# Kernel tuning notes

Hardware: AMD Instinct MI355X
Metric: run time of the kernel (lower is better)

Reference implementation:

```python
import jax, jax.numpy as jnp
import numpy as np

H_DIM = 256
N_HEADS = 8
HALF = H_DIM // 2

def _lin(x, W, b):
    # torch nn.Linear: y = x @ W.T + b
    y = x @ W.T
    return y + b if b is not None else y

def setup_inputs() -> dict:
    key = jax.random.key(0)
    ks = jax.random.split(key, 16)
    s = 0.02
    d = {
        'x': jax.random.normal(ks[0], (16, H_DIM, 32, 32), jnp.float32),
        'q1_w': jax.random.normal(ks[1], (HALF, HALF), jnp.float32) * s,
        'q1_b': jnp.zeros((HALF,), jnp.float32),
        'q2_w': jax.random.normal(ks[2], (HALF, HALF), jnp.float32) * s,
        'q2_b': jnp.zeros((HALF,), jnp.float32),
        'k1_w': jax.random.normal(ks[3], (HALF, HALF), jnp.float32) * s,
        'k1_b': jnp.zeros((HALF,), jnp.float32),
        'k2_w': jax.random.normal(ks[4], (HALF, HALF), jnp.float32) * s,
        'k2_b': jnp.zeros((HALF,), jnp.float32),
        'v1_w': jax.random.normal(ks[5], (HALF, HALF), jnp.float32) * s,
        'v1_b': jnp.zeros((HALF,), jnp.float32),
        'v2_w': jax.random.normal(ks[6], (HALF, HALF), jnp.float32) * s,
        'v2_b': jnp.zeros((HALF,), jnp.float32),
        'proj1_w': jax.random.normal(ks[7], (HALF, HALF), jnp.float32) * s,
        'proj1_b': jnp.zeros((HALF,), jnp.float32),
        'proj2_w': jax.random.normal(ks[8], (HALF, HALF), jnp.float32) * s,
        'proj2_b': jnp.zeros((HALF,), jnp.float32),
        'logit_scale': jnp.log(10.0 * jnp.ones((N_HEADS, 1, 1), jnp.float32)),
        'mlp_w1': jax.random.normal(ks[9], (128, 2), jnp.float32) * s,
        'mlp_b1': jnp.zeros((128,), jnp.float32),
        'mlp_w2': jax.random.normal(ks[10], (N_HEADS, 128), jnp.float32) * s,
    }
    return d

def _rel_pos_index(h, w):
    # static (numpy) relative position index, shape [N, N]
    ch, cw = np.meshgrid(np.arange(h), np.arange(w), indexing='ij')
    coords = np.stack([ch.reshape(-1), cw.reshape(-1)])  # [2, N]
    rel = coords[:, :, None] - coords[:, None, :]         # [2, N, N]
    rel = rel.transpose(1, 2, 0)
    rel[:, :, 0] += h - 1
    rel[:, :, 1] += w - 1
    return rel[:, :, 0] * (2 * w - 1) + rel[:, :, 1]

def _forward(x, q1_w, q1_b, q2_w, q2_b, k1_w, k1_b, k2_w, k2_b,
             v1_w, v1_b, v2_w, v2_b, proj1_w, proj1_b, proj2_w, proj2_b,
             logit_scale, mlp_w1, mlp_b1, mlp_w2):
    b, c, h, w = x.shape
    N = h * w
    nh = N_HEADS
    hd = c // nh
    x3 = jnp.transpose(x, (0, 2, 3, 1)).reshape(b, N, c)
    x0, x1 = x3[..., :c // 2], x3[..., c // 2:]

    def qkv(W0, b0, W1, b1):
        t = jnp.concatenate([x0 + _lin(x0, W0, b0), x1 + _lin(x1, W1, b1)], axis=-1)
        return t.reshape(b, N, nh, hd).transpose(0, 2, 1, 3)  # [b, nh, N, hd]

    q = qkv(q1_w, q1_b, q2_w, q2_b)
    k = qkv(k1_w, k1_b, k2_w, k2_b)
    v = qkv(v1_w, v1_b, v2_w, v2_b)

    eps = 1e-12
    qn = q / jnp.maximum(jnp.linalg.norm(q, axis=-1, keepdims=True), eps)
    kn = k / jnp.maximum(jnp.linalg.norm(k, axis=-1, keepdims=True), eps)
    attn = jnp.einsum('bhnd,bhmd->bhnm', qn, kn)  # cosine similarity
    scale = jnp.exp(jnp.minimum(logit_scale, jnp.log(1.0 / 0.01)))  # [nh,1,1]
    attn = attn * scale[None]

    # continuous relative-position bias (CPB) table via small MLP
    rch = jnp.arange(-(h - 1), h, dtype=jnp.float32) / (h - 1 + 1e-8)
    rcw = jnp.arange(-(w - 1), w, dtype=jnp.float32) / (w - 1 + 1e-8)
    gh, gw = jnp.meshgrid(rch, rcw, indexing='ij')
    tab = jnp.stack([gh, gw], axis=-1) * 3.2               # [2h-1, 2w-1, 2]
    tab = jnp.sign(tab) * (1.0 - jnp.exp(-jnp.abs(tab)))
    tab = jax.nn.relu(_lin(tab, mlp_w1, mlp_b1))
    tab = _lin(tab, mlp_w2, None).reshape(-1, nh)          # [(2h-1)(2w-1), nh]

    idx = jnp.asarray(_rel_pos_index(h, w))                # [N, N]
    bias = tab[idx.reshape(-1)].reshape(N, N, nh).transpose(2, 0, 1)
    bias = 16.0 * jax.nn.sigmoid(bias)
    attn = attn + bias[None]

    attn = jax.nn.softmax(attn, axis=-1)
    out = jnp.einsum('bhnm,bhmd->bhnd', attn, v).transpose(0, 2, 1, 3).reshape(b, N, c)
    o0, o1 = out[..., :c // 2], out[..., c // 2:]
    out = jnp.concatenate([_lin(o0, proj1_w, proj1_b), _lin(o1, proj2_w, proj2_b)], axis=-1)
    return out.reshape(b, h, w, c).transpose(0, 3, 1, 2)

def reference(x, q1_w, q1_b, q2_w, q2_b, k1_w, k1_b, k2_w, k2_b,
              v1_w, v1_b, v2_w, v2_b, proj1_w, proj1_b, proj2_w, proj2_b,
              logit_scale, mlp_w1, mlp_b1, mlp_w2):
    return _forward(x, q1_w, q1_b, q2_w, q2_b, k1_w, k1_b, k2_w, k2_b,
                    v1_w, v1_b, v2_w, v2_b, proj1_w, proj1_b, proj2_w, proj2_b,
                    logit_scale, mlp_w1, mlp_b1, mlp_w2)
```

## Files before the change

### kernel.cpp

```cpp
#include <hip/hip_runtime.h>
#include <cmath>


typedef _Float16 half_t;
typedef __attribute__((ext_vector_type(4))) _Float16 half4;
typedef __attribute__((ext_vector_type(8))) _Float16 half8;
typedef __attribute__((ext_vector_type(4))) float float4v;

static __device__ __forceinline__ float4v mfma16(half8 a, half8 b, float4v c) {
  return __builtin_amdgcn_mfma_f32_16x16x32_f16(a, b, c, 0, 0, 0);
}

struct PtrArr8 { const float* p[8]; };

__global__ __launch_bounds__(256) void bias_mlp(const float* __restrict__ w1,
                                                const float* __restrict__ b1,
                                                const float* __restrict__ w2,
                                                const float* __restrict__ ls,
                                                float* __restrict__ tabh2) {
  __shared__ float sw1[256];
  __shared__ float sb1[128];
  __shared__ float sw2[1024];
  int t = threadIdx.x;
  sw1[t] = w1[t];
  if (t < 128) sb1[t] = b1[t];
  for (int i = t; i < 1024; i += 256) sw2[i] = w2[i];
  __syncthreads();
  int p = blockIdx.x * 256 + t;
  if (p >= 3969) return;
  int ph = p / 63, pw = p % 63;
  float t0 = (float)(ph - 31) * (3.2f / 31.0f);
  float t1 = (float)(pw - 31) * (3.2f / 31.0f);
  t0 = copysignf(1.0f - __expf(-fabsf(t0)), t0);
  t1 = copysignf(1.0f - __expf(-fabsf(t1)), t1);
  float acc[8];
#pragma unroll
  for (int hh = 0; hh < 8; hh++) acc[hh] = 0.0f;
  for (int j = 0; j < 128; j++) {
    float hj = fmaxf(0.0f, t0 * sw1[2 * j] + t1 * sw1[2 * j + 1] + sb1[j]);
#pragma unroll
    for (int hh = 0; hh < 8; hh++) acc[hh] += hj * sw2[hh * 128 + j];
  }
  const float L2E = 1.44269504f;
#pragma unroll
  for (int hh = 0; hh < 8; hh++) {
    float scale = __expf(fminf(ls[hh], 4.6051702f));
    float c14 = 14.0f - (scale + 16.0f) * L2E;
    float bias = 16.0f / (1.0f + __expf(-acc[hh]));
    tabh2[hh * 3969 + p] = bias * L2E + c14;
  }
}

__global__ __launch_bounds__(256) void qkv_mfma(
    const float* __restrict__ x, PtrArr8 wsrc, PtrArr8 bsrc,
    const float* __restrict__ lscale, half_t* __restrict__ qf,
    half_t* __restrict__ kf, half_t* __restrict__ vf) {
  __shared__ half_t wb[128 * 136];
  __shared__ half_t tbuf[128 * 68];
  int t = threadIdx.x;
  int lane = t & 63, wv = t >> 6, l = lane & 15, quad = lane >> 4;
  int hf = blockIdx.y;
  int m0 = blockIdx.x * 64;
  int b = m0 >> 10, n0 = m0 & 1023;

  half8 afr[4];
  {
    const float* xb = x + (size_t)b * 256 * 1024 + n0 + wv * 16 + l;
#pragma unroll
    for (int ks = 0; ks < 4; ks++) {
      int kbase = hf * 128 + ks * 32 + quad * 8;
      half8 a;
#pragma unroll
      for (int j = 0; j < 8; j++)
        a[j] = (half_t)xb[(size_t)(kbase + j) * 1024];
      afr[ks] = a;
    }
  }

  for (int op = 0; op < 3; op++) {
    int combo = op * 2 + hf;
    const float* wg = nullptr;
    const float* bg = nullptr;
#pragma unroll
    for (int i = 0; i < 6; i++)
      if (i == combo) { wg = wsrc.p[i]; bg = bsrc.p[i]; }
    __syncthreads();
#pragma unroll
    for (int i = 0; i < 16; i++) {
      int flat = (t + 256 * i) * 4;
      int row = flat >> 7, col = flat & 127;
      float4 w = *(const float4*)(wg + flat);
      half4 h;
      h[0] = (half_t)(w.x + (col == row ? 1.0f : 0.0f));
      h[1] = (half_t)(w.y + (col + 1 == row ? 1.0f : 0.0f));
      h[2] = (half_t)(w.z + (col + 2 == row ? 1.0f : 0.0f));
      h[3] = (half_t)(w.w + (col + 3 == row ? 1.0f : 0.0f));
      *(half4*)(wb + row * 136 + col) = h;
    }
    __syncthreads();

    float4v acc[8];
#pragma unroll
    for (int ng = 0; ng < 8; ng++) {
      float4v c = {0.f, 0.f, 0.f, 0.f};
#pragma unroll
      for (int ks = 0; ks < 4; ks++) {
        half8 bfrag =
            *(const half8*)(wb + (ng * 16 + l) * 136 + ks * 32 + quad * 8);
        c = mfma16(afr[ks], bfrag, c);
      }
      acc[ng] = c;
    }
#pragma unroll
    for (int ng = 0; ng < 8; ng++) {
      float bb = bg[ng * 16 + l];
#pragma unroll
      for (int r2 = 0; r2 < 4; r2++) acc[ng][r2] += bb;
    }
    if (op < 2) {
#pragma unroll
      for (int hg = 0; hg < 4; hg++) {
        float sc = 1.0f;
        if (op == 0)
          sc = __expf(fminf(lscale[hf * 4 + hg], 4.6051702f)) * 1.44269504f;
#pragma unroll
        for (int r2 = 0; r2 < 4; r2++) {
          float ss = acc[2 * hg][r2] * acc[2 * hg][r2] +
                     acc[2 * hg + 1][r2] * acc[2 * hg + 1][r2];
          ss += __shfl_xor(ss, 1, 64);
          ss += __shfl_xor(ss, 2, 64);
          ss += __shfl_xor(ss, 4, 64);
          ss += __shfl_xor(ss, 8, 64);
          float rn = sc / fmaxf(sqrtf(ss), 1e-12f);
          acc[2 * hg][r2] *= rn;
          acc[2 * hg + 1][r2] *= rn;
        }
      }
#pragma unroll
      for (int ng = 0; ng < 8; ng++)
#pragma unroll
        for (int r2 = 0; r2 < 4; r2++)
          tbuf[(wv * 16 + quad * 4 + r2) * 132 + ng * 16 + l] =
              (half_t)acc[ng][r2];
      __syncthreads();
      half_t* dst = (op == 0) ? qf : kf;
#pragma unroll
      for (int i = 0; i < 4; i++) {
        int idx = t + 256 * i;
        int row = idx >> 4, colc = (idx & 15) * 8;
        half8 vv = *(const half8*)(tbuf + row * 132 + colc);
        int head = hf * 4 + (colc >> 5), d = colc & 31;
        *(half8*)(dst + (((size_t)b * 8 + head) * 1024 + n0 + row) * 32 + d) =
            vv;
      }
    } else {
#pragma unroll
      for (int ng = 0; ng < 8; ng++) {
        int col = ng * 16 + l;
        half4 hv;
#pragma unroll
        for (int r2 = 0; r2 < 4; r2++) hv[r2] = (half_t)acc[ng][r2];
        *(half4*)(tbuf + col * 68 + wv * 16 + quad * 4) = hv;
      }
      __syncthreads();
#pragma unroll
      for (int i = 0; i < 16; i++) {
        int idx = t + 256 * i;
        int col = idx >> 5, rp = idx & 31;
        unsigned int val = *(const unsigned int*)(tbuf + col * 68 + rp * 2);
        int head = hf * 4 + (col >> 5);
        int d = col & 31;
        *(unsigned int*)((char*)vf +
                         (((((size_t)b * 8 + head) * 32 + d) * 1024) + n0 +
                          rp * 2) * 2) = val;
      }
    }
  }
}

__global__ __launch_bounds__(256) void attn_mfma(
    const half_t* __restrict__ qf, const half_t* __restrict__ kf,
    const half_t* __restrict__ vf, const float* __restrict__ tabh2,
    half_t* __restrict__ ao) {
  __shared__ float sb2[35 * 63];
  __shared__ half_t pa[4 * 16 * 80];

  int t = threadIdx.x;
  int lane = t & 63, wv = t >> 6, l = lane & 15, quad = lane >> 4;
  int qo = blockIdx.x, h = blockIdx.y, b = blockIdx.z;
  size_t bh = (size_t)b * 8 + h;
  const half_t* kbase = kf + bh * 1024 * 32;
  const half_t* vbase = vf + bh * 32 * 1024;

  for (int i = t; i < 2205; i += 256)
    sb2[i] = tabh2[h * 3969 + qo * 252 + i];

  int row0 = qo * 128 + wv * 32;
  half8 qfr[2];
#pragma unroll
  for (int s = 0; s < 2; s++)
    qfr[s] =
        *(const half8*)(qf + (bh * 1024 + row0 + s * 16 + l) * 32 + quad * 8);

  float4v o0[2], o1[2];
  float run_l[2];
#pragma unroll
  for (int s = 0; s < 2; s++) {
    o0[s] = (float4v){0.f, 0.f, 0.f, 0.f};
    o1[s] = (float4v){0.f, 0.f, 0.f, 0.f};
    run_l[s] = 0.0f;
  }
  half_t* paw = pa + wv * 16 * 80;
  __syncthreads();

#pragma unroll 2
  for (int kt = 0; kt < 16; kt++) {
    half8 kfr[4], v0fr[2], v1fr[2];
#pragma unroll
    for (int nt = 0; nt < 4; nt++)
      kfr[nt] =
          *(const half8*)(kbase + (kt * 64 + nt * 16 + l) * 32 + quad * 8);
#pragma unroll
    for (int ks = 0; ks < 2; ks++) {
      v0fr[ks] = *(const half8*)(vbase + l * 1024 + kt * 64 + ks * 32 +
                                 quad * 8);
      v1fr[ks] = *(const half8*)(vbase + (16 + l) * 1024 + kt * 64 + ks * 32 +
                                 quad * 8);
    }
#pragma unroll
    for (int s = 0; s < 2; s++) {
      float4v sres[4];
#pragma unroll
      for (int nt = 0; nt < 4; nt++) {
        int base = (wv - 2 * kt - (nt >> 1) + 31) * 63 + s * 16 + l + 31 -
                   (nt & 1) * 16 - quad * 4;
        float4v c;
        c[0] = sb2[base];
        c[1] = sb2[base - 1];
        c[2] = sb2[base - 2];
        c[3] = sb2[base - 3];
        sres[nt] = mfma16(kfr[nt], qfr[s], c);
      }
#pragma unroll
      for (int nt = 0; nt < 4; nt++) {
        half4 ph;
#pragma unroll
        for (int r2 = 0; r2 < 4; r2++) {
          float p = exp2f(sres[nt][r2]);
          run_l[s] += p;
          ph[r2] = (half_t)p;
        }
        *(half4*)(paw + l * 80 + nt * 16 + quad * 4) = ph;
      }
#pragma unroll
      for (int ks = 0; ks < 2; ks++) {
        half8 pfr = *(const half8*)(paw + l * 80 + ks * 32 + quad * 8);
        o0[s] = mfma16(pfr, v0fr[ks], o0[s]);
        o1[s] = mfma16(pfr, v1fr[ks], o1[s]);
      }
    }
  }

#pragma unroll
  for (int s = 0; s < 2; s++) {
    float rl = run_l[s];
    rl += __shfl_xor(rl, 16, 64);
    rl += __shfl_xor(rl, 32, 64);
    float rli = 1.0f / rl;
#pragma unroll
    for (int r2 = 0; r2 < 4; r2++) {
      float linv = __shfl(rli, 20 * quad + r2, 64);
      size_t rowaddr =
          ((size_t)b * 1024 + row0 + s * 16 + quad * 4 + r2) * 256 + h * 32;
      ao[rowaddr + l] = (half_t)(o0[s][r2] * linv);
      ao[rowaddr + 16 + l] = (half_t)(o1[s][r2] * linv);
    }
  }
}

__global__ __launch_bounds__(256) void proj_mfma(
    const half_t* __restrict__ ao, PtrArr8 wsrc, PtrArr8 bsrc,
    float* __restrict__ out) {
  __shared__ half_t wb[128 * 136];
  __shared__ float yt[128 * 68];
  int t = threadIdx.x;
  int lane = t & 63, wv = t >> 6, l = lane & 15, quad = lane >> 4;
  int hf = blockIdx.y;
  int m0 = blockIdx.x * 64;
  int b = m0 >> 10, n0 = m0 & 1023;

  const float* wg = hf ? wsrc.p[7] : wsrc.p[6];
  const float* bg = hf ? bsrc.p[7] : bsrc.p[6];
#pragma unroll
  for (int i = 0; i < 16; i++) {
    int flat = (t + 256 * i) * 4;
    int row = flat >> 7, col = flat & 127;
    float4 w = *(const float4*)(wg + flat);
    half4 h;
    h[0] = (half_t)w.x;
    h[1] = (half_t)w.y;
    h[2] = (half_t)w.z;
    h[3] = (half_t)w.w;
    *(half4*)(wb + row * 136 + col) = h;
  }

  half8 afr[4];
  const half_t* ab =
      ao + ((size_t)m0 + wv * 16 + l) * 256 + hf * 128 + quad * 8;
#pragma unroll
  for (int ks = 0; ks < 4; ks++) afr[ks] = *(const half8*)(ab + ks * 32);
  __syncthreads();

#pragma unroll
  for (int ng = 0; ng < 8; ng++) {
    float4v c = {0.f, 0.f, 0.f, 0.f};
#pragma unroll
    for (int ks = 0; ks < 4; ks++)
      c = mfma16(afr[ks],
                 *(const half8*)(wb + (ng * 16 + l) * 136 + ks * 32 +
                                 quad * 8),
                 c);
    float bb = bg[ng * 16 + l];
#pragma unroll
    for (int r2 = 0; r2 < 4; r2++) c[r2] += bb;
    *(float4v*)(yt + (ng * 16 + l) * 68 + wv * 16 + quad * 4) = c;
  }
  __syncthreads();
#pragma unroll
  for (int i = 0; i < 8; i++) {
    int idx = t + 256 * i;
    int col = idx >> 4, rg = idx & 15;
    float4v vv = *(const float4v*)(yt + col * 68 + rg * 4);
    *(float4v*)(out + ((size_t)b * 256 + hf * 128 + col) * 1024 + n0 +
                rg * 4) = vv;
  }
}

extern "C" void kernel_launch(void* const* d_in, const int* in_sizes, int n_in,
                              void* d_out, int out_size, void* d_ws,
                              size_t ws_size, hipStream_t stream) {
  (void)in_sizes; (void)n_in; (void)out_size; (void)ws_size;
  const float* x = (const float*)d_in[0];

  half_t* ws = (half_t*)d_ws;
  half_t* qfp = ws;
  half_t* kfp = ws + 4194304;
  half_t* vfp = ws + 8388608;
  half_t* aop = ws + 12582912;
  float* tabh2 = (float*)((char*)d_ws + 33816576);

  PtrArr8 wsrc, bsrc;
  const int widx[8] = {1, 3, 5, 7, 9, 11, 13, 15};
  for (int i = 0; i < 8; i++) {
    wsrc.p[i] = (const float*)d_in[widx[i]];
    bsrc.p[i] = (const float*)d_in[widx[i] + 1];
  }

  bias_mlp<<<16, 256, 0, stream>>>((const float*)d_in[18],
                                   (const float*)d_in[19],
                                   (const float*)d_in[20],
                                   (const float*)d_in[17], tabh2);
  qkv_mfma<<<dim3(256, 2), 256, 0, stream>>>(x, wsrc, bsrc,
                                             (const float*)d_in[17], qfp, kfp,
                                             vfp);
  attn_mfma<<<dim3(8, 8, 16), 256, 0, stream>>>(qfp, kfp, vfp, tabh2, aop);
  proj_mfma<<<dim3(256, 2), 256, 0, stream>>>(aop, wsrc, bsrc, (float*)d_out);
}
```

Baseline: 226.2 us.

## Pre-pack weights into MFMA fragment layout and halve row tiles in QKV/proj

Result: faster. 188.1 us (-16.8%).

```diff
diff --git a/kernel.cpp b/kernel.cpp
--- a/kernel.cpp
+++ b/kernel.cpp
@@ -12,6 +12,36 @@
 }
 
 struct PtrArr8 { const float* p[8]; };
+
+__global__ __launch_bounds__(256) void prep_w(PtrArr8 wsrc, PtrArr8 bsrc,
+                                              half_t* __restrict__ wf,
+                                              float* __restrict__ bws) {
+  int y = blockIdx.y;
+  const float* src = nullptr;
+  const float* bs = nullptr;
+#pragma unroll
+  for (int i = 0; i < 8; i++)
+    if (i == y) { src = wsrc.p[i]; bs = bsrc.p[i]; }
+  int flat = (blockIdx.x * 256 + threadIdx.x) * 4;
+  float4 w = *(const float4*)(src + flat);
+  int j = flat >> 7, k = flat & 127;
+  if (y < 6) {
+    if (k == j)     w.x += 1.0f;
+    if (k + 1 == j) w.y += 1.0f;
+    if (k + 2 == j) w.z += 1.0f;
+    if (k + 3 == j) w.w += 1.0f;
+  }
+  half4 h;
+  h[0] = (half_t)w.x;
+  h[1] = (half_t)w.y;
+  h[2] = (half_t)w.z;
+  h[3] = (half_t)w.w;
+  int ng = j >> 4, l = j & 15, ks = k >> 5, quad = (k >> 3) & 3, o8 = k & 7;
+  *(half4*)(wf + y * 16384 + ((ng * 4 + ks) * 64 + quad * 16 + l) * 8 + o8) =
+      h;
+  if (blockIdx.x == 0 && threadIdx.x < 128)
+    bws[y * 128 + threadIdx.x] = bs[threadIdx.x];
+}
 
 __global__ __launch_bounds__(256) void bias_mlp(const float* __restrict__ w1,
                                                 const float* __restrict__ b1,
@@ -51,123 +81,108 @@
   }
 }
 
-__global__ __launch_bounds__(256) void qkv_mfma(
-    const float* __restrict__ x, PtrArr8 wsrc, PtrArr8 bsrc,
-    const float* __restrict__ lscale, half_t* __restrict__ qf,
-    half_t* __restrict__ kf, half_t* __restrict__ vf) {
-  __shared__ half_t wb[128 * 136];
-  __shared__ half_t tbuf[128 * 68];
+__global__ __launch_bounds__(256, 4) void qkv_mfma(
+    const float* __restrict__ x, const half_t* __restrict__ wfrag,
+    const float* __restrict__ lscale, const float* __restrict__ bws,
+    half_t* __restrict__ qf, half_t* __restrict__ kf,
+    half_t* __restrict__ vf) {
+  __shared__ half_t tbuf[4608];
   int t = threadIdx.x;
   int lane = t & 63, wv = t >> 6, l = lane & 15, quad = lane >> 4;
+  int rw = wv & 1, cw = wv >> 1;
   int hf = blockIdx.y;
-  int m0 = blockIdx.x * 64;
+  int m0 = blockIdx.x * 32;
   int b = m0 >> 10, n0 = m0 & 1023;
 
   half8 afr[4];
   {
-    const float* xb = x + (size_t)b * 256 * 1024 + n0 + wv * 16 + l;
+    const float* xb =
+        x + ((size_t)b * 256 + hf * 128) * 1024 + n0 + rw * 16 + l;
 #pragma unroll
     for (int ks = 0; ks < 4; ks++) {
-      int kbase = hf * 128 + ks * 32 + quad * 8;
       half8 a;
 #pragma unroll
       for (int j = 0; j < 8; j++)
-        a[j] = (half_t)xb[(size_t)(kbase + j) * 1024];
+        a[j] = (half_t)xb[(size_t)(ks * 32 + quad * 8 + j) * 1024];
       afr[ks] = a;
     }
   }
 
   for (int op = 0; op < 3; op++) {
     int combo = op * 2 + hf;
-    const float* wg = nullptr;
-    const float* bg = nullptr;
-#pragma unroll
-    for (int i = 0; i < 6; i++)
-      if (i == combo) { wg = wsrc.p[i]; bg = bsrc.p[i]; }
-    __syncthreads();
-#pragma unroll
-    for (int i = 0; i < 16; i++) {
-      int flat = (t + 256 * i) * 4;
-      int row = flat >> 7, col = flat & 127;
-      float4 w = *(const float4*)(wg + flat);
-      half4 h;
-      h[0] = (half_t)(w.x + (col == row ? 1.0f : 0.0f));
-      h[1] = (half_t)(w.y + (col + 1 == row ? 1.0f : 0.0f));
-      h[2] = (half_t)(w.z + (col + 2 == row ? 1.0f : 0.0f));
-      h[3] = (half_t)(w.w + (col + 3 == row ? 1.0f : 0.0f));
-      *(half4*)(wb + row * 136 + col) = h;
-    }
-    __syncthreads();
-
-    float4v acc[8];
-#pragma unroll
-    for (int ng = 0; ng < 8; ng++) {
+    const half_t* wfb = wfrag + combo * 16384;
+    float4v acc[4];
+#pragma unroll
+    for (int ngl = 0; ngl < 4; ngl++) {
+      int ng = cw * 4 + ngl;
       float4v c = {0.f, 0.f, 0.f, 0.f};
 #pragma unroll
       for (int ks = 0; ks < 4; ks++) {
         half8 bfrag =
-            *(const half8*)(wb + (ng * 16 + l) * 136 + ks * 32 + quad * 8);
+            *(const half8*)(wfb + ((ng * 4 + ks) * 64 + lane) * 8);
         c = mfma16(afr[ks], bfrag, c);
       }
-      acc[ng] = c;
-    }
-#pragma unroll
-    for (int ng = 0; ng < 8; ng++) {
-      float bb = bg[ng * 16 + l];
-#pragma unroll
-      for (int r2 = 0; r2 < 4; r2++) acc[ng][r2] += bb;
+      acc[ngl] = c;
+    }
+#pragma unroll
+    for (int ngl = 0; ngl < 4; ngl++) {
+      float bb = bws[combo * 128 + (cw * 4 + ngl) * 16 + l];
+#pragma unroll
+      for (int r2 = 0; r2 < 4; r2++) acc[ngl][r2] += bb;
     }
     if (op < 2) {
 #pragma unroll
-      for (int hg = 0; hg < 4; hg++) {
+      for (int hgl = 0; hgl < 2; hgl++) {
         float sc = 1.0f;
         if (op == 0)
-          sc = __expf(fminf(lscale[hf * 4 + hg], 4.6051702f)) * 1.44269504f;
+          sc = __expf(fminf(lscale[hf * 4 + cw * 2 + hgl], 4.6051702f)) *
+               1.44269504f;
 #pragma unroll
         for (int r2 = 0; r2 < 4; r2++) {
-          float ss = acc[2 * hg][r2] * acc[2 * hg][r2] +
-                     acc[2 * hg + 1][r2] * acc[2 * hg + 1][r2];
+          float ss = acc[2 * hgl][r2] * acc[2 * hgl][r2] +
+                     acc[2 * hgl + 1][r2] * acc[2 * hgl + 1][r2];
           ss += __shfl_xor(ss, 1, 64);
           ss += __shfl_xor(ss, 2, 64);
           ss += __shfl_xor(ss, 4, 64);
           ss += __shfl_xor(ss, 8, 64);
           float rn = sc / fmaxf(sqrtf(ss), 1e-12f);
-          acc[2 * hg][r2] *= rn;
-          acc[2 * hg + 1][r2] *= rn;
+          acc[2 * hgl][r2] *= rn;
+          acc[2 * hgl + 1][r2] *= rn;
         }
       }
 #pragma unroll
-      for (int ng = 0; ng < 8; ng++)
+      for (int ngl = 0; ngl < 4; ngl++)
 #pragma unroll
         for (int r2 = 0; r2 < 4; r2++)
-          tbuf[(wv * 16 + quad * 4 + r2) * 132 + ng * 16 + l] =
-              (half_t)acc[ng][r2];
+          tbuf[(rw * 16 + quad * 4 + r2) * 136 + (cw * 4 + ngl) * 16 + l] =
+              (half_t)acc[ngl][r2];
       __syncthreads();
       half_t* dst = (op == 0) ? qf : kf;
 #pragma unroll
-      for (int i = 0; i < 4; i++) {
+      for (int i = 0; i < 2; i++) {
         int idx = t + 256 * i;
         int row = idx >> 4, colc = (idx & 15) * 8;
-        half8 vv = *(const half8*)(tbuf + row * 132 + colc);
+        half8 vv = *(const half8*)(tbuf + row * 136 + colc);
         int head = hf * 4 + (colc >> 5), d = colc & 31;
         *(half8*)(dst + (((size_t)b * 8 + head) * 1024 + n0 + row) * 32 + d) =
             vv;
       }
+      __syncthreads();
     } else {
 #pragma unroll
-      for (int ng = 0; ng < 8; ng++) {
-        int col = ng * 16 + l;
+      for (int ngl = 0; ngl < 4; ngl++) {
+        int col = (cw * 4 + ngl) * 16 + l;
         half4 hv;
 #pragma unroll
-        for (int r2 = 0; r2 < 4; r2++) hv[r2] = (half_t)acc[ng][r2];
-        *(half4*)(tbuf + col * 68 + wv * 16 + quad * 4) = hv;
+        for (int r2 = 0; r2 < 4; r2++) hv[r2] = (half_t)acc[ngl][r2];
+        *(half4*)(tbuf + col * 36 + rw * 16 + quad * 4) = hv;
       }
       __syncthreads();
 #pragma unroll
-      for (int i = 0; i < 16; i++) {
+      for (int i = 0; i < 8; i++) {
         int idx = t + 256 * i;
-        int col = idx >> 5, rp = idx & 31;
-        unsigned int val = *(const unsigned int*)(tbuf + col * 68 + rp * 2);
+        int col = idx >> 4, rp = idx & 15;
+        unsigned int val = *(const unsigned int*)(tbuf + col * 36 + rp * 2);
         int head = hf * 4 + (col >> 5);
         int d = col & 31;
         *(unsigned int*)((char*)vf +
@@ -185,12 +200,15 @@
   __shared__ float sb2[35 * 63];
   __shared__ half_t pa[4 * 16 * 80];
 
+  int id = blockIdx.x;
+  int qo = id >> 7;
+  int bh = id & 127;
+  int h = bh & 7, b = bh >> 3;
   int t = threadIdx.x;
   int lane = t & 63, wv = t >> 6, l = lane & 15, quad = lane >> 4;
-  int qo = blockIdx.x, h = blockIdx.y, b = blockIdx.z;
-  size_t bh = (size_t)b * 8 + h;
-  const half_t* kbase = kf + bh * 1024 * 32;
-  const half_t* vbase = vf + bh * 32 * 1024;
+  size_t bhs = (size_t)b * 8 + h;
+  const half_t* kbase = kf + bhs * 1024 * 32;
+  const half_t* vbase = vf + bhs * 32 * 1024;
 
   for (int i = t; i < 2205; i += 256)
     sb2[i] = tabh2[h * 3969 + qo * 252 + i];
@@ -199,8 +217,8 @@
   half8 qfr[2];
 #pragma unroll
   for (int s = 0; s < 2; s++)
-    qfr[s] =
-        *(const half8*)(qf + (bh * 1024 + row0 + s * 16 + l) * 32 + quad * 8);
+    qfr[s] = *(const half8*)(qf + (bhs * 1024 + row0 + s * 16 + l) * 32 +
+                             quad * 8);
 
   float4v o0[2], o1[2];
   float run_l[2];
@@ -278,59 +296,44 @@
   }
 }
 
-__global__ __launch_bounds__(256) void proj_mfma(
-    const half_t* __restrict__ ao, PtrArr8 wsrc, PtrArr8 bsrc,
-    float* __restrict__ out) {
-  __shared__ half_t wb[128 * 136];
-  __shared__ float yt[128 * 68];
+__global__ __launch_bounds__(256, 4) void proj_mfma(
+    const half_t* __restrict__ ao, const half_t* __restrict__ wfrag,
+    const float* __restrict__ bws, float* __restrict__ out) {
+  __shared__ float yt[128 * 36];
   int t = threadIdx.x;
   int lane = t & 63, wv = t >> 6, l = lane & 15, quad = lane >> 4;
+  int rw = wv & 1, cw = wv >> 1;
   int hf = blockIdx.y;
-  int m0 = blockIdx.x * 64;
+  int m0 = blockIdx.x * 32;
   int b = m0 >> 10, n0 = m0 & 1023;
-
-  const float* wg = hf ? wsrc.p[7] : wsrc.p[6];
-  const float* bg = hf ? bsrc.p[7] : bsrc.p[6];
-#pragma unroll
-  for (int i = 0; i < 16; i++) {
-    int flat = (t + 256 * i) * 4;
-    int row = flat >> 7, col = flat & 127;
-    float4 w = *(const float4*)(wg + flat);
-    half4 h;
-    h[0] = (half_t)w.x;
-    h[1] = (half_t)w.y;
-    h[2] = (half_t)w.z;
-    h[3] = (half_t)w.w;
-    *(half4*)(wb + row * 136 + col) = h;
-  }
 
   half8 afr[4];
   const half_t* ab =
-      ao + ((size_t)m0 + wv * 16 + l) * 256 + hf * 128 + quad * 8;
+      ao + ((size_t)m0 + rw * 16 + l) * 256 + hf * 128 + quad * 8;
 #pragma unroll
   for (int ks = 0; ks < 4; ks++) afr[ks] = *(const half8*)(ab + ks * 32);
+
+  const half_t* wfb = wfrag + (6 + hf) * 16384;
+#pragma unroll
+  for (int ngl = 0; ngl < 4; ngl++) {
+    int ng = cw * 4 + ngl;
+    float4v c = {0.f, 0.f, 0.f, 0.f};
+#pragma unroll
+    for (int ks = 0; ks < 4; ks++) {
+      half8 bfrag = *(const half8*)(wfb + ((ng * 4 + ks) * 64 + lane) * 8);
+      c = mfma16(afr[ks], bfrag, c);
+    }
+    float bb = bws[(6 + hf) * 128 + ng * 16 + l];
+#pragma unroll
+    for (int r2 = 0; r2 < 4; r2++) c[r2] += bb;
+    *(float4v*)(yt + (ng * 16 + l) * 36 + rw * 16 + quad * 4) = c;
+  }
   __syncthreads();
-
-#pragma unroll
-  for (int ng = 0; ng < 8; ng++) {
-    float4v c = {0.f, 0.f, 0.f, 0.f};
-#pragma unroll
-    for (int ks = 0; ks < 4; ks++)
-      c = mfma16(afr[ks],
-                 *(const half8*)(wb + (ng * 16 + l) * 136 + ks * 32 +
-                                 quad * 8),
-                 c);
-    float bb = bg[ng * 16 + l];
-#pragma unroll
-    for (int r2 = 0; r2 < 4; r2++) c[r2] += bb;
-    *(float4v*)(yt + (ng * 16 + l) * 68 + wv * 16 + quad * 4) = c;
-  }
-  __syncthreads();
-#pragma unroll
-  for (int i = 0; i < 8; i++) {
+#pragma unroll
+  for (int i = 0; i < 4; i++) {
     int idx = t + 256 * i;
-    int col = idx >> 4, rg = idx & 15;
-    float4v vv = *(const float4v*)(yt + col * 68 + rg * 4);
+    int col = idx >> 3, rg = idx & 7;
+    float4v vv = *(const float4v*)(yt + col * 36 + rg * 4);
     *(float4v*)(out + ((size_t)b * 256 + hf * 128 + col) * 1024 + n0 +
                 rg * 4) = vv;
   }
@@ -347,7 +350,9 @@
   half_t* kfp = ws + 4194304;
   half_t* vfp = ws + 8388608;
   half_t* aop = ws + 12582912;
+  half_t* wfp = ws + 16777216;
   float* tabh2 = (float*)((char*)d_ws + 33816576);
+  float* bws = (float*)((char*)d_ws + 33943584);
 
   PtrArr8 wsrc, bsrc;
   const int widx[8] = {1, 3, 5, 7, 9, 11, 13, 15};
@@ -356,13 +361,13 @@
     bsrc.p[i] = (const float*)d_in[widx[i] + 1];
   }
 
+  prep_w<<<dim3(16, 8), 256, 0, stream>>>(wsrc, bsrc, wfp, bws);
   bias_mlp<<<16, 256, 0, stream>>>((const float*)d_in[18],
                                    (const float*)d_in[19],
                                    (const float*)d_in[20],
                                    (const float*)d_in[17], tabh2);
-  qkv_mfma<<<dim3(256, 2), 256, 0, stream>>>(x, wsrc, bsrc,
-                                             (const float*)d_in[17], qfp, kfp,
-                                             vfp);
-  attn_mfma<<<dim3(8, 8, 16), 256, 0, stream>>>(qfp, kfp, vfp, tabh2, aop);
-  proj_mfma<<<dim3(256, 2), 256, 0, stream>>>(aop, wsrc, bsrc, (float*)d_out);
-}
+  qkv_mfma<<<dim3(512, 2), 256, 0, stream>>>(x, wfp, (const float*)d_in[17],
+                                             bws, qfp, kfp, vfp);
+  attn_mfma<<<1024, 256, 0, stream>>>(qfp, kfp, vfp, tabh2, aop);
+  proj_mfma<<<dim3(512, 2), 256, 0, stream>>>(aop, wfp, bws, (float*)d_out);
+}
```
